# Kernel tuning notes

Measured on AMD Instinct MI355X. Metric: run time of the kernel, lower is better.

Reference implementation:

```python
import jax, jax.numpy as jnp
import numpy as np

B, S, D, H = 2, 2048, 1024, 16
DK = D // H  # 64


def setup_inputs() -> dict:
    key = jax.random.key(0)
    ks = jax.random.split(key, 5)
    std = 0.02
    return {
        "x": jax.random.normal(ks[0], (B, S, D), dtype=jnp.float32),
        "Wq": jax.random.normal(ks[1], (D, D), dtype=jnp.float32) * std,
        "bq": jnp.zeros((D,), jnp.float32),
        "Wk": jax.random.normal(ks[2], (D, D), dtype=jnp.float32) * std,
        "bk": jnp.zeros((D,), jnp.float32),
        "Wv": jax.random.normal(ks[3], (D, D), dtype=jnp.float32) * std,
        "bv": jnp.zeros((D,), jnp.float32),
        "Wo": jax.random.normal(ks[4], (D, D), dtype=jnp.float32) * std,
        "bo": jnp.zeros((D,), jnp.float32),
    }


def reference(x, Wq, bq, Wk, bk, Wv, bv, Wo, bo):
    b, s, d = x.shape
    # QKV projections (torch Linear: x @ W.T + b)
    q = x @ Wq.T + bq
    k = x @ Wk.T + bk
    v = x @ Wv.T + bv
    # [b, s, d] -> [b, h, s, d_k]
    q = q.reshape(b, s, H, DK).transpose(0, 2, 1, 3)
    k = k.reshape(b, s, H, DK).transpose(0, 2, 1, 3)
    v = v.reshape(b, s, H, DK).transpose(0, 2, 1, 3)
    # scaled dot-product scores [b, h, s, s]
    scores = jnp.einsum('bhqd,bhkd->bhqk', q, k) / np.float32(np.sqrt(DK))
    # causal mask (mask=True path in original forward)
    causal = jnp.tril(jnp.ones((s, s), dtype=bool))
    scores = jnp.where(causal, scores, jnp.float32(-1e9))
    attn = jax.nn.softmax(scores, axis=-1)
    # dropout is identity in eval / p=0
    out = jnp.einsum('bhqk,bhkd->bhqd', attn, v)
    out = out.transpose(0, 2, 1, 3).reshape(b, s, d)
    return out @ Wo.T + bo
```

## Files before the change

### kernel.cpp

```cpp
#include <hip/hip_runtime.h>
#include <stdint.h>
#include <math.h>

#define B_ 2
#define S_ 2048
#define D_ 1024
#define H_ 16
#define DK_ 64
#define M_ (B_*S_)
#define NT_ 16

typedef unsigned short u16;
typedef unsigned int u32;
typedef __attribute__((ext_vector_type(8))) __bf16 bf16x8;
typedef __attribute__((ext_vector_type(4))) float f32x4;

#define AS1 __attribute__((address_space(1)))
#define AS3 __attribute__((address_space(3)))

__device__ __forceinline__ u16 f2bf(float f) {
  u32 u = __float_as_uint(f);
  return (u16)((u + 0x7fffu + ((u >> 16) & 1u)) >> 16);
}
__device__ __forceinline__ u16 f2bfr(float f) {
  return (u16)((__float_as_uint(f) + 0x8000u) >> 16);
}

__device__ __forceinline__ void gload_lds16(const void* g, void* lds) {
  __builtin_amdgcn_global_load_lds((const AS1 u32*)g,
                                   (AS3 u32*)(u32)(uintptr_t)lds, 16, 0, 0);
}

__device__ __forceinline__ f32x4 mfma16(bf16x8 a, bf16x8 b, f32x4 c) {
  return __builtin_amdgcn_mfma_f32_16x16x32_bf16(a, b, c, 0, 0, 0);
}

#define VMCNT_(n) asm volatile("s_waitcnt vmcnt(" #n ")" ::: "memory")
#define VMCNT(n) VMCNT_(n)

__global__ __launch_bounds__(256) void f2bf_kernel(const float* __restrict__ in,
                                                   u16* __restrict__ out, int n4) {
  int i = blockIdx.x * 256 + threadIdx.x;
  if (i >= n4) return;
  float4 v = ((const float4*)in)[i];
  u32 lo = (u32)f2bf(v.x) | ((u32)f2bf(v.y) << 16);
  u32 hi = (u32)f2bf(v.z) | ((u32)f2bf(v.w) << 16);
  ((uint2*)out)[i] = make_uint2(lo, hi);
}

__global__ __launch_bounds__(256) void f2bf4_kernel(
    const float* __restrict__ W0, const float* __restrict__ W1,
    const float* __restrict__ W2, const float* __restrict__ W3,
    u16* __restrict__ o0, u16* __restrict__ o1, u16* __restrict__ o2, u16* __restrict__ o3,
    int n4) {
  const float* src; u16* dst;
  switch (blockIdx.y) {
    case 0: src = W0; dst = o0; break;
    case 1: src = W1; dst = o1; break;
    case 2: src = W2; dst = o2; break;
    default: src = W3; dst = o3; break;
  }
  int i = blockIdx.x * 256 + threadIdx.x;
  if (i >= n4) return;
  float4 v = ((const float4*)src)[i];
  u32 lo = (u32)f2bf(v.x) | ((u32)f2bf(v.y) << 16);
  u32 hi = (u32)f2bf(v.z) | ((u32)f2bf(v.w) << 16);
  ((uint2*)dst)[i] = make_uint2(lo, hi);
}

__global__ __launch_bounds__(512, 1) void gemm_qkv_8ph(
    const u16* __restrict__ A,
    const u16* __restrict__ W0, const u16* __restrict__ W1, const u16* __restrict__ W2,
    const float* __restrict__ b0, const float* __restrict__ b1, const float* __restrict__ b2,
    u16* __restrict__ C0, u16* __restrict__ C1, u16* __restrict__ C2) {
  const int id = blockIdx.x;
  const int xcd = id & 7, k = id >> 3;
  const int my = xcd*2 + (k & 1);
  const int rest = k >> 1;
  const int z = rest >> 2, nx = rest & 3;

  const u16* W = (z == 0) ? W0 : (z == 1) ? W1 : W2;
  const float* bias = (z == 0) ? b0 : (z == 1) ? b1 : b2;
  u16* C = (z == 0) ? C0 : (z == 1) ? C1 : C2;
  const float osc = (z == 0) ? 0.18033688f : 1.0f;
  const int mbase = my*256, nbase = nx*256;

  __shared__ u16 LA[2][256*64];
  __shared__ u16 LB[2][256*64];

  const int tid = threadIdx.x;
  const int w = tid >> 6, lane = tid & 63;
  const int lo = lane & 15, hi = lane >> 4;
  const int wr = w >> 2, wc = w & 3;

  const int sr = tid >> 3;
  const int sc = tid & 7;
  const int sx = (sc ^ (sr & 7)) * 8;

#define STAGE_A(buf, t, h) do {                                                   \
    int gr_ = sr + (h)*64;                                                        \
    size_t g_ = (size_t)(mbase + gr_)*D_ + (size_t)(t)*64 + sx;                   \
    gload_lds16(&A[g_],            &LA[buf][gr_*64 + sc*8]);                      \
    gload_lds16(&A[g_ + 128*D_],   &LA[buf][(gr_ + 128)*64 + sc*8]);              \
  } while (0)

#define STAGE_B(buf, t, h) do {                                                   \
    int gr_ = (sr & 31) + (h)*32 + (sr >> 5)*64;                                  \
    size_t g_ = (size_t)(nbase + gr_)*D_ + (size_t)(t)*64 + sx;                   \
    gload_lds16(&W[g_],            &LB[buf][gr_*64 + sc*8]);                      \
    gload_lds16(&W[g_ + 128*D_],   &LB[buf][(gr_ + 128)*64 + sc*8]);              \
  } while (0)

  f32x4 acc[8][4] = {};

#define PHASE(buf, mq, nq, STAGE_STMT, WAIT_STMT) do {                            \
    bf16x8 af_[4][2], bv_[2][2];                                                  \
    _Pragma("unroll")                                                             \
    for (int m_ = 0; m_ < 4; ++m_) {                                              \
      int R_ = wr*128 + (mq)*64 + m_*16 + lo;                                     \
      int rx_ = R_ & 7, base_ = R_*64;                                            \
      af_[m_][0] = *(const bf16x8*)&LA[buf][base_ + ((hi ^ rx_) * 8)];            \
      af_[m_][1] = *(const bf16x8*)&LA[buf][base_ + (((4 + hi) ^ rx_) * 8)];      \
    }                                                                             \
    _Pragma("unroll")                                                             \
    for (int n_ = 0; n_ < 2; ++n_) {                                              \
      int R_ = wc*64 + (nq)*32 + n_*16 + lo;                                      \
      int rx_ = R_ & 7, base_ = R_*64;                                            \
      bv_[n_][0] = *(const bf16x8*)&LB[buf][base_ + ((hi ^ rx_) * 8)];            \
      bv_[n_][1] = *(const bf16x8*)&LB[buf][base_ + (((4 + hi) ^ rx_) * 8)];      \
    }                                                                             \
    STAGE_STMT;                                                                   \
    WAIT_STMT;                                                                    \
    __builtin_amdgcn_s_barrier();                                                 \
    __builtin_amdgcn_s_setprio(1);                                                \
    _Pragma("unroll")                                                             \
    for (int m_ = 0; m_ < 4; ++m_)                                                \
      _Pragma("unroll")                                                           \
      for (int n_ = 0; n_ < 2; ++n_) {                                            \
        acc[(mq)*4 + m_][(nq)*2 + n_] =                                           \
            mfma16(af_[m_][0], bv_[n_][0], acc[(mq)*4 + m_][(nq)*2 + n_]);        \
        acc[(mq)*4 + m_][(nq)*2 + n_] =                                           \
            mfma16(af_[m_][1], bv_[n_][1], acc[(mq)*4 + m_][(nq)*2 + n_]);        \
      }                                                                           \
    __builtin_amdgcn_s_setprio(0);                                                \
    __builtin_amdgcn_s_barrier();                                                 \
  } while (0)

  STAGE_A(0, 0, 0); STAGE_B(0, 0, 0);
  STAGE_A(0, 0, 1); STAGE_B(0, 0, 1);
  STAGE_A(1, 1, 0); STAGE_B(1, 1, 0);
  VMCNT(8);
  __builtin_amdgcn_s_barrier();

  for (int j = 0; j < NT_/2; ++j) {
    const int t1 = 2*j + 1;
    const int tp0 = (2*j + 2 < NT_) ? 2*j + 2 : NT_ - 1;
    const int tp1 = (2*j + 3 < NT_) ? 2*j + 3 : NT_ - 1;
    PHASE(0, 0, 0, STAGE_A(1, t1, 1),  VMCNT(6));
    PHASE(0, 0, 1, STAGE_B(1, t1, 1),  (void)0);
    PHASE(0, 1, 0, STAGE_A(0, tp0, 0), (void)0);
    PHASE(0, 1, 1, STAGE_B(0, tp0, 0), VMCNT(8));
    PHASE(1, 0, 0, STAGE_A(0, tp0, 1), VMCNT(6));
    PHASE(1, 0, 1, STAGE_B(0, tp0, 1), (void)0);
    PHASE(1, 1, 0, STAGE_A(1, tp1, 0), (void)0);
    PHASE(1, 1, 1, STAGE_B(1, tp1, 0), VMCNT(8));
  }

#pragma unroll
  for (int n = 0; n < 4; ++n) {
    int col = nbase + wc*64 + n*16 + lo;
    float bv2 = bias[col];
#pragma unroll
    for (int m = 0; m < 8; ++m)
#pragma unroll
      for (int jj = 0; jj < 4; ++jj) {
        int row = mbase + wr*128 + m*16 + hi*4 + jj;
        C[(size_t)row*D_ + col] = f2bf((acc[m][n][jj] + bv2) * osc);
      }
  }
#undef PHASE
#undef STAGE_A
#undef STAGE_B
}

__global__ __launch_bounds__(256) void gemm_bt64(
    const u16* __restrict__ A, const u16* __restrict__ W,
    const float* __restrict__ bias, float* __restrict__ C,
    int M, int N, int K) {
  __shared__ u16 As[64*32];
  __shared__ u16 Bs[128*32];
  const int tid = threadIdx.x;
  const int wave = tid >> 6, lane = tid & 63;
  const int lo = lane & 15, hi = lane >> 4;
  const int mbase = blockIdx.y * 64, nbase = blockIdx.x * 128;

  f32x4 acc[4][2] = {};

  for (int k0 = 0; k0 < K; k0 += 32) {
    {
      int row = tid >> 2;
      int col = (tid & 3) * 8;
      gload_lds16(&A[(size_t)(mbase + row)*K + k0 + col], &As[row*32 + col]);
#pragma unroll
      for (int i = 0; i < 2; ++i)
        gload_lds16(&W[(size_t)(nbase + i*64 + row)*K + k0 + col], &Bs[(i*64 + row)*32 + col]);
    }
    __syncthreads();
    bf16x8 af[4], bfr[2];
#pragma unroll
    for (int m = 0; m < 4; ++m)
      af[m] = *(const bf16x8*)&As[(m*16 + lo)*32 + hi*8];
#pragma unroll
    for (int n = 0; n < 2; ++n)
      bfr[n] = *(const bf16x8*)&Bs[(wave*32 + n*16 + lo)*32 + hi*8];
#pragma unroll
    for (int m = 0; m < 4; ++m)
#pragma unroll
      for (int n = 0; n < 2; ++n)
        acc[m][n] = __builtin_amdgcn_mfma_f32_16x16x32_bf16(af[m], bfr[n], acc[m][n], 0, 0, 0);
    __syncthreads();
  }

#pragma unroll
  for (int n = 0; n < 2; ++n) {
    int col = nbase + wave*32 + n*16 + lo;
    float bv = bias[col];
#pragma unroll
    for (int m = 0; m < 4; ++m)
#pragma unroll
      for (int j = 0; j < 4; ++j) {
        int row = mbase + m*16 + hi*4 + j;
        C[(size_t)row*N + col] = acc[m][n][j] + bv;
      }
  }
}

__global__ __launch_bounds__(256) void transpose_v(const u16* __restrict__ V,
                                                   u16* __restrict__ Vt) {
  const int st = blockIdx.x, bh = blockIdx.y;
  const int b = bh >> 4, h = bh & 15;
  __shared__ u16 tile[64][72];
  const int tid = threadIdx.x;
#pragma unroll
  for (int c = 0; c < 2; ++c) {
    int s = c*32 + (tid >> 3);
    int d0 = (tid & 7) * 8;
    *(uint4*)&tile[s][d0] =
        *(const uint4*)&V[((size_t)(b*S_ + st*64 + s))*D_ + h*DK_ + d0];
  }
  __syncthreads();
#pragma unroll
  for (int c = 0; c < 2; ++c) {
    int d = c*32 + (tid >> 3);
    int s0 = (tid & 7) * 8;
    uint4 ov;
    u16* tp = (u16*)&ov;
#pragma unroll
    for (int jj = 0; jj < 8; ++jj) tp[jj] = tile[s0 + jj][d];
    *(uint4*)&Vt[((size_t)(bh*DK_ + d))*S_ + st*64 + s0] = ov;
  }
}

__global__ __launch_bounds__(256) void attn_kernel(
    const u16* __restrict__ Q, const u16* __restrict__ K, const u16* __restrict__ Vt,
    u16* __restrict__ AO) {
  const int blk = blockIdx.x;
  const int xcd = blk & 7, slot = blk >> 3;
  const int bh = xcd + 8*(slot & 3);
  const int qt = 31 - (slot >> 2);
  const int b = bh >> 4, h = bh & 15;
  const int tid = threadIdx.x, w = tid >> 6, lane = tid & 63;
  const int lo = lane & 15, hi = lane >> 4;

  __shared__ u16 Kl[2][64*64];
  __shared__ u16 Vl[2][64*64];
  __shared__ u16 Pl[4][16*72];

  const int r8 = lane >> 3;
  const int rloc = w*8 + r8;
  const int xorcol = ((lane & 7) ^ r8) * 8;
  const size_t kbase = (size_t)b*S_*D_ + (size_t)h*DK_;
  const size_t vbase = (size_t)bh*DK_*S_;
  const size_t koff0 = kbase + (size_t)rloc*D_ + xorcol;
  const size_t koff1 = kbase + (size_t)(32 + rloc)*D_ + xorcol;
  const size_t voff0 = vbase + (size_t)rloc*S_ + xorcol;
  const size_t voff1 = vbase + (size_t)(32 + rloc)*S_ + xorcol;
  const int ldsoff = rloc*64 + (lane & 7)*8;

  const int qrow = qt*64 + w*16 + lo;
  bf16x8 qf[2];
#pragma unroll
  for (int kk = 0; kk < 2; ++kk)
    qf[kk] = *(const bf16x8*)&Q[(size_t)(b*S_ + qrow)*D_ + h*DK_ + kk*32 + hi*8];

  f32x4 o[4] = {};
  float mr = -INFINITY, lr = 0.f;

  gload_lds16(&K[koff0], &Kl[0][ldsoff]);
  gload_lds16(&K[koff1], &Kl[0][2048 + ldsoff]);
  gload_lds16(&Vt[voff0], &Vl[0][ldsoff]);
  gload_lds16(&Vt[voff1], &Vl[0][2048 + ldsoff]);

  for (int kt = 0; kt <= qt; ++kt) {
    const int cur = kt & 1;
    __syncthreads();
    if (kt < qt) {
      const size_t kadd = (size_t)(kt + 1)*64*D_;
      const int vadd = (kt + 1)*64;
      gload_lds16(&K[koff0 + kadd], &Kl[cur ^ 1][ldsoff]);
      gload_lds16(&K[koff1 + kadd], &Kl[cur ^ 1][2048 + ldsoff]);
      gload_lds16(&Vt[voff0 + vadd], &Vl[cur ^ 1][ldsoff]);
      gload_lds16(&Vt[voff1 + vadd], &Vl[cur ^ 1][2048 + ldsoff]);
    }

    f32x4 s[4] = {};
#pragma unroll
    for (int kk = 0; kk < 2; ++kk) {
#pragma unroll
      for (int n = 0; n < 4; ++n) {
        int row = n*16 + lo;
        bf16x8 kf = *(const bf16x8*)&Kl[cur][row*64 + (((kk*4 + hi) ^ (row & 7)) * 8)];
        s[n] = __builtin_amdgcn_mfma_f32_16x16x32_bf16(kf, qf[kk], s[n], 0, 0, 0);
      }
    }

    if (kt == qt) {
      const int ql = w*16 + lo;
#pragma unroll
      for (int n = 0; n < 4; ++n)
#pragma unroll
        for (int j = 0; j < 4; ++j)
          if (n*16 + hi*4 + j > ql) s[n][j] = -INFINITY;
    }

    float pm = -INFINITY;
#pragma unroll
    for (int n = 0; n < 4; ++n)
#pragma unroll
      for (int j = 0; j < 4; ++j) pm = fmaxf(pm, s[n][j]);

    if (!__all(pm <= mr + 11.0f)) {
      pm = fmaxf(pm, __shfl_xor(pm, 16));
      pm = fmaxf(pm, __shfl_xor(pm, 32));
      float mn = fmaxf(mr, pm);
      float corr = __builtin_amdgcn_exp2f(mr - mn);
      mr = mn;
      lr *= corr;
      float cj[4];
#pragma unroll
      for (int j = 0; j < 4; ++j) cj[j] = __shfl(corr, hi*4 + j);
#pragma unroll
      for (int n = 0; n < 4; ++n)
#pragma unroll
        for (int j = 0; j < 4; ++j) o[n][j] *= cj[j];
    }

#pragma unroll
    for (int n = 0; n < 4; ++n) {
      float p0 = __builtin_amdgcn_exp2f(s[n][0] - mr);
      float p1 = __builtin_amdgcn_exp2f(s[n][1] - mr);
      float p2 = __builtin_amdgcn_exp2f(s[n][2] - mr);
      float p3 = __builtin_amdgcn_exp2f(s[n][3] - mr);
      lr += (p0 + p1) + (p2 + p3);
      u32 d01 = (u32)f2bfr(p0) | ((u32)f2bfr(p1) << 16);
      u32 d23 = (u32)f2bfr(p2) | ((u32)f2bfr(p3) << 16);
      *(uint2*)&Pl[w][lo*72 + n*16 + hi*4] = make_uint2(d01, d23);
    }

#pragma unroll
    for (int kk = 0; kk < 2; ++kk) {
      bf16x8 pf = *(const bf16x8*)&Pl[w][lo*72 + kk*32 + hi*8];
#pragma unroll
      for (int n = 0; n < 4; ++n) {
        int row = n*16 + lo;
        bf16x8 vf = *(const bf16x8*)&Vl[cur][row*64 + (((kk*4 + hi) ^ (row & 7)) * 8)];
        o[n] = __builtin_amdgcn_mfma_f32_16x16x32_bf16(pf, vf, o[n], 0, 0, 0);
      }
    }
  }

  lr += __shfl_xor(lr, 16);
  lr += __shfl_xor(lr, 32);
  float rinv[4];
#pragma unroll
  for (int j = 0; j < 4; ++j) rinv[j] = __builtin_amdgcn_rcpf(__shfl(lr, hi*4 + j));
#pragma unroll
  for (int n = 0; n < 4; ++n)
#pragma unroll
    for (int j = 0; j < 4; ++j) {
      int rowg = qt*64 + w*16 + hi*4 + j;
      AO[(size_t)(b*S_ + rowg)*D_ + h*DK_ + n*16 + lo] = f2bf(o[n][j] * rinv[j]);
    }
}

extern "C" void kernel_launch(void* const* d_in, const int* in_sizes, int n_in,
                              void* d_out, int out_size, void* d_ws, size_t ws_size,
                              hipStream_t stream) {
  const float* x  = (const float*)d_in[0];
  const float* Wq = (const float*)d_in[1];
  const float* bq = (const float*)d_in[2];
  const float* Wk = (const float*)d_in[3];
  const float* bk = (const float*)d_in[4];
  const float* Wv = (const float*)d_in[5];
  const float* bv = (const float*)d_in[6];
  const float* Wo = (const float*)d_in[7];
  const float* bo = (const float*)d_in[8];

  char* ws = (char*)d_ws;
  const size_t MB = 1048576;
  u16* xb  = (u16*)(ws + 0);
  u16* Wqb = (u16*)(ws + 8*MB);
  u16* Wkb = (u16*)(ws + 10*MB);
  u16* Wvb = (u16*)(ws + 12*MB);
  u16* Wob = (u16*)(ws + 14*MB);
  u16* Qb  = (u16*)(ws + 16*MB);
  u16* Kb  = (u16*)(ws + 24*MB);
  u16* Vb  = (u16*)(ws + 32*MB);
  u16* Vtb = (u16*)(ws + 0);
  u16* AOb = (u16*)(ws + 32*MB);

  f2bf_kernel<<<4096, 256, 0, stream>>>(x, xb, (M_*D_)/4);
  f2bf4_kernel<<<dim3(1024, 4), 256, 0, stream>>>(Wq, Wk, Wv, Wo,
                                                  Wqb, Wkb, Wvb, Wob, (D_*D_)/4);

  gemm_qkv_8ph<<<192, 512, 0, stream>>>(xb, Wqb, Wkb, Wvb, bq, bk, bv, Qb, Kb, Vb);

  transpose_v<<<dim3(32, 32), 256, 0, stream>>>(Vb, Vtb);

  attn_kernel<<<1024, 256, 0, stream>>>(Qb, Kb, Vtb, AOb);

  gemm_bt64<<<dim3(8, 64), 256, 0, stream>>>(AOb, Wob, bo, (float*)d_out, M_, D_, D_);
}
```

Before: 114.6 us.

## Restructure QKV GEMM into K-split four-phase tiles with reused B fragments

Replaces the eight-phase per-quadrant schedule with a four-phase-per-tile schedule that splits each 64-wide K slice into two halves. B fragments for each K half are loaded once and reused across both M halves, which cuts LDS reads. Global-to-LDS staging and vmcnt waits are reordered to match. Launch bounds are also raised to request two blocks per CU. That adds register pressure from holding two sets of B fragments and risks spills, and LDS use (128 KB per block) may still allow only one block per CU.

```diff
diff --git a/kernel.cpp b/kernel.cpp
--- a/kernel.cpp
+++ b/kernel.cpp
@@ -68,7 +68,7 @@
   ((uint2*)dst)[i] = make_uint2(lo, hi);
 }
 
-__global__ __launch_bounds__(512, 1) void gemm_qkv_8ph(
+__global__ __launch_bounds__(512, 2) void gemm_qkv_8ph(
     const u16* __restrict__ A,
     const u16* __restrict__ W0, const u16* __restrict__ W1, const u16* __restrict__ W2,
     const float* __restrict__ b0, const float* __restrict__ b1, const float* __restrict__ b2,
@@ -111,59 +111,75 @@
     gload_lds16(&W[g_ + 128*D_],   &LB[buf][(gr_ + 128)*64 + sc*8]);              \
   } while (0)
 
-  f32x4 acc[8][4] = {};
-
-#define PHASE(buf, mq, nq, STAGE_STMT, WAIT_STMT) do {                            \
-    bf16x8 af_[4][2], bv_[2][2];                                                  \
+#define LDA_F(dst, buf, mq, kk) do {                                              \
     _Pragma("unroll")                                                             \
     for (int m_ = 0; m_ < 4; ++m_) {                                              \
       int R_ = wr*128 + (mq)*64 + m_*16 + lo;                                     \
-      int rx_ = R_ & 7, base_ = R_*64;                                            \
-      af_[m_][0] = *(const bf16x8*)&LA[buf][base_ + ((hi ^ rx_) * 8)];            \
-      af_[m_][1] = *(const bf16x8*)&LA[buf][base_ + (((4 + hi) ^ rx_) * 8)];      \
+      dst[m_] = *(const bf16x8*)&LA[buf][R_*64 + ((((kk)*4 + hi) ^ (R_ & 7))*8)]; \
     }                                                                             \
+  } while (0)
+
+#define LDB_F(dst, buf, kk) do {                                                  \
     _Pragma("unroll")                                                             \
-    for (int n_ = 0; n_ < 2; ++n_) {                                              \
-      int R_ = wc*64 + (nq)*32 + n_*16 + lo;                                      \
-      int rx_ = R_ & 7, base_ = R_*64;                                            \
-      bv_[n_][0] = *(const bf16x8*)&LB[buf][base_ + ((hi ^ rx_) * 8)];            \
-      bv_[n_][1] = *(const bf16x8*)&LB[buf][base_ + (((4 + hi) ^ rx_) * 8)];      \
-    }                                                                             \
-    STAGE_STMT;                                                                   \
-    WAIT_STMT;                                                                    \
-    __builtin_amdgcn_s_barrier();                                                 \
+    for (int q_ = 0; q_ < 2; ++q_)                                                \
+      _Pragma("unroll")                                                           \
+      for (int n_ = 0; n_ < 2; ++n_) {                                            \
+        int R_ = wc*64 + q_*32 + n_*16 + lo;                                      \
+        dst[q_][n_] =                                                             \
+            *(const bf16x8*)&LB[buf][R_*64 + ((((kk)*4 + hi) ^ (R_ & 7))*8)];     \
+      }                                                                           \
+  } while (0)
+
+#define MM(mq, af_, bv_) do {                                                     \
     __builtin_amdgcn_s_setprio(1);                                                \
     _Pragma("unroll")                                                             \
     for (int m_ = 0; m_ < 4; ++m_)                                                \
       _Pragma("unroll")                                                           \
-      for (int n_ = 0; n_ < 2; ++n_) {                                            \
-        acc[(mq)*4 + m_][(nq)*2 + n_] =                                           \
-            mfma16(af_[m_][0], bv_[n_][0], acc[(mq)*4 + m_][(nq)*2 + n_]);        \
-        acc[(mq)*4 + m_][(nq)*2 + n_] =                                           \
-            mfma16(af_[m_][1], bv_[n_][1], acc[(mq)*4 + m_][(nq)*2 + n_]);        \
-      }                                                                           \
+      for (int q_ = 0; q_ < 2; ++q_)                                              \
+        _Pragma("unroll")                                                         \
+        for (int n_ = 0; n_ < 2; ++n_)                                            \
+          acc[(mq)*4 + m_][q_*2 + n_] =                                           \
+              mfma16(af_[m_], bv_[q_][n_], acc[(mq)*4 + m_][q_*2 + n_]);          \
     __builtin_amdgcn_s_setprio(0);                                                \
-    __builtin_amdgcn_s_barrier();                                                 \
+  } while (0)
+
+#define BAR __builtin_amdgcn_s_barrier()
+
+  f32x4 acc[8][4] = {};
+
+#define TILE(buf, t) do {                                                         \
+    const int tn1_ = ((t) + 1 < NT_) ? (t) + 1 : NT_ - 1;                         \
+    const int tn2_ = ((t) + 2 < NT_) ? (t) + 2 : NT_ - 1;                         \
+    bf16x8 af[4], bv0[2][2], bv1[2][2];                                           \
+                                                              \
+    LDA_F(af, buf, 0, 0); LDB_F(bv0, buf, 0);                                     \
+    STAGE_B(1 - (buf), tn1_, 1);                                                  \
+    BAR; MM(0, af, bv0); BAR;                                                     \
+                                                              \
+    LDA_F(af, buf, 0, 1); LDB_F(bv1, buf, 1);                                     \
+    STAGE_A(1 - (buf), tn1_, 1);                                                  \
+    VMCNT(8);                                                                     \
+    BAR; MM(0, af, bv1); BAR;                                                     \
+                                                 \
+    LDA_F(af, buf, 1, 0);                                                         \
+    STAGE_A(buf, tn2_, 0);                                                        \
+    BAR; MM(1, af, bv0); BAR;                                                     \
+                                                 \
+    LDA_F(af, buf, 1, 1);                                                         \
+    STAGE_B(buf, tn2_, 0);                                                        \
+    VMCNT(6);                                                                     \
+    BAR; MM(1, af, bv1); BAR;                                                     \
   } while (0)
 
   STAGE_A(0, 0, 0); STAGE_B(0, 0, 0);
-  STAGE_A(0, 0, 1); STAGE_B(0, 0, 1);
+  STAGE_B(0, 0, 1); STAGE_A(0, 0, 1);
   STAGE_A(1, 1, 0); STAGE_B(1, 1, 0);
-  VMCNT(8);
-  __builtin_amdgcn_s_barrier();
+  VMCNT(6);
+  BAR;
 
   for (int j = 0; j < NT_/2; ++j) {
-    const int t1 = 2*j + 1;
-    const int tp0 = (2*j + 2 < NT_) ? 2*j + 2 : NT_ - 1;
-    const int tp1 = (2*j + 3 < NT_) ? 2*j + 3 : NT_ - 1;
-    PHASE(0, 0, 0, STAGE_A(1, t1, 1),  VMCNT(6));
-    PHASE(0, 0, 1, STAGE_B(1, t1, 1),  (void)0);
-    PHASE(0, 1, 0, STAGE_A(0, tp0, 0), (void)0);
-    PHASE(0, 1, 1, STAGE_B(0, tp0, 0), VMCNT(8));
-    PHASE(1, 0, 0, STAGE_A(0, tp0, 1), VMCNT(6));
-    PHASE(1, 0, 1, STAGE_B(0, tp0, 1), (void)0);
-    PHASE(1, 1, 0, STAGE_A(1, tp1, 0), (void)0);
-    PHASE(1, 1, 1, STAGE_B(1, tp1, 0), VMCNT(8));
+    TILE(0, 2*j);
+    TILE(1, 2*j + 1);
   }
 
 #pragma unroll
@@ -178,9 +194,13 @@
         C[(size_t)row*D_ + col] = f2bf((acc[m][n][jj] + bv2) * osc);
       }
   }
-#undef PHASE
+#undef TILE
+#undef MM
+#undef LDA_F
+#undef LDB_F
 #undef STAGE_A
 #undef STAGE_B
+#undef BAR
 }
 
 __global__ __launch_bounds__(256) void gemm_bt64(
```

Measured after the change: 110.0 us. -4.0%, faster.
